# Optimization experiments

Hardware: AMD Instinct MI355X
Metric: run time of the kernel (lower is better)

Reference implementation:

```python
import jax, jax.numpy as jnp
import numpy as np

IN_DIM = 768
HID = 1024          # d_model of Mamba2
CLIP = 512
NG = 4              # ngroups
DS = 64             # d_state
DC = 4              # d_conv
HD = 64             # headdim (Mamba2 default)
DIN = 2 * HID       # d_inner (expand=2)
NH = DIN // HD      # nheads = 32
CONV_DIM = DIN + 2 * NG * DS          # 2560
DINP = 2 * DIN + 2 * NG * DS + NH     # 4640 (d_mlp = 0)
BATCH = 1024
EPS = 1e-5


def setup_inputs() -> dict:
    key = jax.random.key(0)
    ks = jax.random.split(key, 12)
    r = lambda i, shape, s=0.02: jax.random.normal(ks[i], shape, jnp.float32) * s
    return {
        "frame_feat": jax.random.normal(ks[0], (BATCH, IN_DIM), jnp.float32),
        "conv_state": jax.random.normal(ks[1], (BATCH, CONV_DIM, DC), jnp.float32) * 0.1,
        "ssm_state": jax.random.normal(ks[2], (BATCH, NH, HD, DS), jnp.float32) * 0.1,
        "ln_w": jnp.ones((IN_DIM,), jnp.float32),
        "ln_b": jnp.zeros((IN_DIM,), jnp.float32),
        "w_in_gate": r(3, (HID, IN_DIM)),
        "b_in_gate": jnp.zeros((HID,), jnp.float32),
        "w_input_proj": r(4, (HID, IN_DIM)),
        "b_input_proj": jnp.zeros((HID,), jnp.float32),
        "w_in_proj": r(5, (DINP, HID)),                 # Mamba2.in_proj (no bias)
        "conv_w": r(6, (CONV_DIM, DC), 0.1),            # conv1d.weight (d,1,w)->(d,w)
        "conv_b": jnp.zeros((CONV_DIM,), jnp.float32),
        "A_log": jnp.log(jnp.arange(1, NH + 1, dtype=jnp.float32)),
        "Dp": jnp.ones((NH,), jnp.float32),
        "dt_bias": r(7, (NH,), 0.5),
        "norm_w": jnp.ones((DIN,), jnp.float32),        # RMSNormGated weight
        "w_out_proj": r(8, (HID, DIN)),                 # Mamba2.out_proj (no bias)
        "w_out_gate": r(9, (HID, HID)),
        "b_out_gate": jnp.zeros((HID,), jnp.float32),
        "w_proj": r(10, (CLIP, HID)),
        "b_proj": jnp.zeros((CLIP,), jnp.float32),
    }


def reference(frame_feat, conv_state, ssm_state, ln_w, ln_b, w_in_gate, b_in_gate,
              w_input_proj, b_input_proj, w_in_proj, conv_w, conv_b, A_log, Dp,
              dt_bias, norm_w, w_out_proj, w_out_gate, b_out_gate, w_proj, b_proj):
    # ---- pre-LayerNorm ----
    mu = jnp.mean(frame_feat, -1, keepdims=True)
    var = jnp.mean((frame_feat - mu) ** 2, -1, keepdims=True)
    x = (frame_feat - mu) * jax.lax.rsqrt(var + EPS) * ln_w + ln_b
    # ---- gated input projection ----
    gated = (x @ w_input_proj.T + b_input_proj) * jax.nn.sigmoid(x @ w_in_gate.T + b_in_gate)
    # ---- Mamba2.step ----
    zxbcdt = gated @ w_in_proj.T                              # (b, DINP)
    z = zxbcdt[:, :DIN]
    xBC = zxbcdt[:, DIN:DIN + CONV_DIM]
    dt = zxbcdt[:, DIN + CONV_DIM:]                           # (b, NH)
    # causal-conv state update (roll left, append, depthwise dot over window)
    new_conv = jnp.concatenate([conv_state[:, :, 1:], xBC[:, :, None]], axis=-1)
    xBC = jax.nn.silu(jnp.sum(new_conv * conv_w, axis=-1) + conv_b)
    xs = xBC[:, :DIN]
    Bs = xBC[:, DIN:DIN + NG * DS]
    Cs = xBC[:, DIN + NG * DS:]
    # selective state update
    A = -jnp.exp(A_log)                                       # (NH,)
    dt = jax.nn.softplus(dt + dt_bias)                        # (b, NH)
    dA = jnp.exp(dt * A)                                      # (b, NH)
    xh = xs.reshape(-1, NH, HD)                               # (b, h, p)
    hpg = NH // NG
    Bh = jnp.repeat(Bs.reshape(-1, NG, DS), hpg, axis=1)      # (b, h, n)
    Ch = jnp.repeat(Cs.reshape(-1, NG, DS), hpg, axis=1)
    new_ssm = ssm_state * dA[:, :, None, None] + (dt[:, :, None] * xh)[..., None] * Bh[:, :, None, :]
    y = jnp.einsum('bhpn,bhn->bhp', new_ssm, Ch) + Dp[None, :, None] * xh
    # gated group RMSNorm (group_size = DIN // NG, gate applied before norm)
    y = y.reshape(-1, DIN) * jax.nn.silu(z)
    yg = y.reshape(-1, NG, DIN // NG)
    yg = yg * jax.lax.rsqrt(jnp.mean(yg * yg, -1, keepdims=True) + EPS)
    y = yg.reshape(-1, DIN) * norm_w
    ssm_out = y @ w_out_proj.T                                # (b, HID)
    # ---- residual + output gate + projection ----
    out = ssm_out + gated
    out = out * jax.nn.sigmoid(out @ w_out_gate.T + b_out_gate)
    clip_emb = out @ w_proj.T + b_proj
    return clip_emb, new_conv, new_ssm
```

## Files before the change

### kernel.cpp

```cpp
#include <hip/hip_runtime.h>
#include <hip/hip_bf16.h>
#include <math.h>

constexpr int B       = 1024;
constexpr int IN_DIM  = 768;
constexpr int HID     = 1024;
constexpr int CLIP    = 512;
constexpr int NG      = 4;
constexpr int DS      = 64;
constexpr int HD      = 64;
constexpr int DIN     = 2 * HID;
constexpr int NH      = DIN / HD;
constexpr int CONV_DIM = DIN + 2 * NG * DS;
constexpr int DINP    = 2 * DIN + 2 * NG * DS + NH;
constexpr float EPS   = 1e-5f;

__device__ __forceinline__ float sigmoidf_(float v) { return 1.f / (1.f + expf(-v)); }

__global__ __launch_bounds__(256) void ln_kernel(
    const float* __restrict__ in, const float* __restrict__ w,
    const float* __restrict__ bvec, float* __restrict__ out)
{
    int row = blockIdx.x, t = threadIdx.x;
    __shared__ float rs[4], rss[4], stats[2];
    float v[3];
    float s = 0.f, ss = 0.f;
#pragma unroll
    for (int i = 0; i < 3; i++) {
        v[i] = in[row * IN_DIM + i * 256 + t];
        s += v[i]; ss += v[i] * v[i];
    }
    for (int o = 32; o; o >>= 1) { s += __shfl_down(s, o); ss += __shfl_down(ss, o); }
    if ((t & 63) == 0) { rs[t >> 6] = s; rss[t >> 6] = ss; }
    __syncthreads();
    if (t == 0) {
        float S = rs[0] + rs[1] + rs[2] + rs[3];
        float SS = rss[0] + rss[1] + rss[2] + rss[3];
        float mu = S * (1.f / IN_DIM);
        float var = SS * (1.f / IN_DIM) - mu * mu;
        stats[0] = mu; stats[1] = rsqrtf(var + EPS);
    }
    __syncthreads();
    float mu = stats[0], r = stats[1];
#pragma unroll
    for (int i = 0; i < 3; i++) {
        int c = i * 256 + t;
        out[row * IN_DIM + c] = (v[i] - mu) * r * w[c] + bvec[c];
    }
}

template <int EPI>
__global__ __launch_bounds__(256) void gemm_kernel(
    const float* __restrict__ A, const float* __restrict__ W,
    const float* __restrict__ bias, const float* __restrict__ other,
    float* __restrict__ C, int M, int N, int K)
{
    __shared__ float As[16][64];
    __shared__ float Ws[16][64];
    int t = threadIdx.x;
    int tx = t & 15, ty = t >> 4;
    int bm = blockIdx.y * 64, bn = blockIdx.x * 64;
    int lr = t >> 2;
    int lk = (t & 3) * 4;
    const float* Aptr = A + (size_t)(bm + lr) * K + lk;
    const float* Wptr = W + (size_t)(bn + lr) * K + lk;
    bool wvalid = (bn + lr) < N;
    float acc[4][4] = {};
    for (int k0 = 0; k0 < K; k0 += 16) {
        float4 av = *(const float4*)(Aptr + k0);
        float4 wv = wvalid ? *(const float4*)(Wptr + k0) : make_float4(0.f, 0.f, 0.f, 0.f);
        __syncthreads();
        As[lk + 0][lr] = av.x; As[lk + 1][lr] = av.y; As[lk + 2][lr] = av.z; As[lk + 3][lr] = av.w;
        Ws[lk + 0][lr] = wv.x; Ws[lk + 1][lr] = wv.y; Ws[lk + 2][lr] = wv.z; Ws[lk + 3][lr] = wv.w;
        __syncthreads();
#pragma unroll
        for (int kk = 0; kk < 16; kk++) {
            float4 a = *(const float4*)&As[kk][ty * 4];
            float4 b = *(const float4*)&Ws[kk][tx * 4];
            acc[0][0] = fmaf(a.x, b.x, acc[0][0]); acc[0][1] = fmaf(a.x, b.y, acc[0][1]);
            acc[0][2] = fmaf(a.x, b.z, acc[0][2]); acc[0][3] = fmaf(a.x, b.w, acc[0][3]);
            acc[1][0] = fmaf(a.y, b.x, acc[1][0]); acc[1][1] = fmaf(a.y, b.y, acc[1][1]);
            acc[1][2] = fmaf(a.y, b.z, acc[1][2]); acc[1][3] = fmaf(a.y, b.w, acc[1][3]);
            acc[2][0] = fmaf(a.z, b.x, acc[2][0]); acc[2][1] = fmaf(a.z, b.y, acc[2][1]);
            acc[2][2] = fmaf(a.z, b.z, acc[2][2]); acc[2][3] = fmaf(a.z, b.w, acc[2][3]);
            acc[3][0] = fmaf(a.w, b.x, acc[3][0]); acc[3][1] = fmaf(a.w, b.y, acc[3][1]);
            acc[3][2] = fmaf(a.w, b.z, acc[3][2]); acc[3][3] = fmaf(a.w, b.w, acc[3][3]);
        }
    }
    int cn = bn + tx * 4;
    if (cn < N) {
        float4 bz = bias ? *(const float4*)(bias + cn) : make_float4(0.f, 0.f, 0.f, 0.f);
#pragma unroll
        for (int i = 0; i < 4; i++) {
            int rm = bm + ty * 4 + i;
            size_t off = (size_t)rm * N + cn;
            float4 r = make_float4(acc[i][0] + bz.x, acc[i][1] + bz.y,
                                   acc[i][2] + bz.z, acc[i][3] + bz.w);
            if (EPI == 1) {
                float4 o = *(const float4*)(other + off);
                r.x *= sigmoidf_(o.x); r.y *= sigmoidf_(o.y);
                r.z *= sigmoidf_(o.z); r.w *= sigmoidf_(o.w);
            } else if (EPI == 2) {
                float4 o = *(const float4*)(other + off);
                r.x += o.x; r.y += o.y; r.z += o.z; r.w += o.w;
            } else if (EPI == 3) {
                float4 o = *(const float4*)(other + off);
                r.x = o.x * sigmoidf_(r.x); r.y = o.y * sigmoidf_(r.y);
                r.z = o.z * sigmoidf_(r.z); r.w = o.w * sigmoidf_(r.w);
            }
            *(float4*)(C + off) = r;
        }
    }
}

__global__ __launch_bounds__(256) void conv_kernel(
    const float* __restrict__ conv_state, const float* __restrict__ zxbcdt,
    const float* __restrict__ cw, const float* __restrict__ cb,
    float* __restrict__ newconv, float* __restrict__ xbcp)
{
    int idx = blockIdx.x * 256 + threadIdx.x;
    int b = idx / CONV_DIM, c = idx - b * CONV_DIM;
    float4 cs = ((const float4*)conv_state)[idx];
    float xin = zxbcdt[(size_t)b * DINP + DIN + c];
    float4 nc = make_float4(cs.y, cs.z, cs.w, xin);
    ((float4*)newconv)[idx] = nc;
    float4 w = ((const float4*)cw)[c];
    float s = nc.x * w.x + nc.y * w.y + nc.z * w.z + nc.w * w.w + cb[c];
    xbcp[idx] = s * sigmoidf_(s);
}

__global__ __launch_bounds__(256) void dt_kernel(
    const float* __restrict__ zxbcdt, const float* __restrict__ dt_bias,
    const float* __restrict__ A_log, float* __restrict__ dtb, float* __restrict__ dab)
{
    int idx = blockIdx.x * 256 + threadIdx.x;
    int b = idx >> 5, h = idx & 31;
    float raw = zxbcdt[(size_t)b * DINP + DIN + CONV_DIM + h] + dt_bias[h];
    float sp = (raw > 20.f) ? raw : log1pf(expf(raw));
    float A = -expf(A_log[h]);
    dtb[idx] = sp;
    dab[idx] = expf(sp * A);
}

__global__ __launch_bounds__(256) void ssm_kernel(
    const float* __restrict__ ssm_state, const float* __restrict__ xbcp,
    const float* __restrict__ dtb, const float* __restrict__ dab,
    const float* __restrict__ Dp, float* __restrict__ newssm, float* __restrict__ ypre)
{
    int bid = blockIdx.x;
    int b = bid >> 5, h = bid & 31, g = h >> 3;
    int t = threadIdx.x;
    __shared__ float xsh[64];
    __shared__ float4 Bsh[16], Csh[16];
    __shared__ float sc[3];
    if (t < 64) xsh[t] = xbcp[(size_t)b * CONV_DIM + h * 64 + t];
    else if (t < 80)  Bsh[t - 64] = ((const float4*)(xbcp + (size_t)b * CONV_DIM + DIN + g * 64))[t - 64];
    else if (t < 96)  Csh[t - 80] = ((const float4*)(xbcp + (size_t)b * CONV_DIM + DIN + NG * DS + g * 64))[t - 80];
    else if (t == 96) sc[0] = dtb[bid];
    else if (t == 97) sc[1] = dab[bid];
    else if (t == 98) sc[2] = Dp[h];
    __syncthreads();
    float sdt = sc[0], sdA = sc[1], sDp = sc[2];
    const float4* sin4 = (const float4*)ssm_state + (size_t)bid * 1024;
    float4* sout4 = (float4*)newssm + (size_t)bid * 1024;
#pragma unroll
    for (int i = 0; i < 4; i++) {
        int idx = i * 256 + t;
        int p = idx >> 4, n4 = idx & 15;
        float4 s = sin4[idx];
        float4 Bv = Bsh[n4], Cv = Csh[n4];
        float coef = sdt * xsh[p];
        float4 ns;
        ns.x = fmaf(s.x, sdA, coef * Bv.x);
        ns.y = fmaf(s.y, sdA, coef * Bv.y);
        ns.z = fmaf(s.z, sdA, coef * Bv.z);
        ns.w = fmaf(s.w, sdA, coef * Bv.w);
        sout4[idx] = ns;
        float part = ns.x * Cv.x + ns.y * Cv.y + ns.z * Cv.z + ns.w * Cv.w;
        for (int o = 8; o; o >>= 1) part += __shfl_down(part, o);
        if ((t & 15) == 0) ypre[(size_t)b * DIN + h * 64 + p] = part + sDp * xsh[p];
    }
}

__global__ __launch_bounds__(128) void gn_kernel(
    const float* __restrict__ ypre, const float* __restrict__ zxbcdt,
    const float* __restrict__ nw, float* __restrict__ yfin)
{
    int bg = blockIdx.x;
    int b = bg >> 2, g = bg & 3;
    int t = threadIdx.x;
    int col = g * 512 + t * 4;
    float4 yv = *(const float4*)(ypre + (size_t)b * DIN + col);
    float4 zv = *(const float4*)(zxbcdt + (size_t)b * DINP + col);
    float4 y2;
    y2.x = yv.x * zv.x * sigmoidf_(zv.x);
    y2.y = yv.y * zv.y * sigmoidf_(zv.y);
    y2.z = yv.z * zv.z * sigmoidf_(zv.z);
    y2.w = yv.w * zv.w * sigmoidf_(zv.w);
    float ss = y2.x * y2.x + y2.y * y2.y + y2.z * y2.z + y2.w * y2.w;
    for (int o = 32; o; o >>= 1) ss += __shfl_down(ss, o);
    __shared__ float red[2]; __shared__ float rfac;
    if ((t & 63) == 0) red[t >> 6] = ss;
    __syncthreads();
    if (t == 0) rfac = rsqrtf((red[0] + red[1]) * (1.f / 512.f) + EPS);
    __syncthreads();
    float r = rfac;
    float4 w4 = *(const float4*)(nw + col);
    float4 o4 = make_float4(y2.x * r * w4.x, y2.y * r * w4.y, y2.z * r * w4.z, y2.w * r * w4.w);
    *(float4*)(yfin + (size_t)b * DIN + col) = o4;
}

extern "C" void kernel_launch(void* const* d_in, const int* in_sizes, int n_in,
                              void* d_out, int out_size, void* d_ws, size_t ws_size,
                              hipStream_t stream)
{
    const float* frame_feat   = (const float*)d_in[0];
    const float* conv_state   = (const float*)d_in[1];
    const float* ssm_state    = (const float*)d_in[2];
    const float* ln_w         = (const float*)d_in[3];
    const float* ln_b         = (const float*)d_in[4];
    const float* w_in_gate    = (const float*)d_in[5];
    const float* b_in_gate    = (const float*)d_in[6];
    const float* w_input_proj = (const float*)d_in[7];
    const float* b_input_proj = (const float*)d_in[8];
    const float* w_in_proj    = (const float*)d_in[9];
    const float* conv_w       = (const float*)d_in[10];
    const float* conv_b       = (const float*)d_in[11];
    const float* A_log        = (const float*)d_in[12];
    const float* Dp           = (const float*)d_in[13];
    const float* dt_bias      = (const float*)d_in[14];
    const float* norm_w       = (const float*)d_in[15];
    const float* w_out_proj   = (const float*)d_in[16];
    const float* w_out_gate   = (const float*)d_in[17];
    const float* b_out_gate   = (const float*)d_in[18];
    const float* w_proj       = (const float*)d_in[19];
    const float* b_proj       = (const float*)d_in[20];

    float* ws = (float*)d_ws;
    float* x      = ws + 0;
    float* g1     = ws + 786432;
    float* gated  = ws + 1835008;
    float* zxbcdt = ws + 2883584;
    float* xbcp   = ws + 7634944;
    float* dtb    = ws + 10256384;
    float* dab    = ws + 10289152;
    float* ypre   = ws + 10321920;
    float* yfin   = ws + 12419072;
    float* outpre = ws + 14516224;
    float* outv   = ws + 15564800;

    float* out     = (float*)d_out;
    float* clip    = out;
    float* newconv = out + (size_t)B * CLIP;
    float* newssm  = newconv + (size_t)B * CONV_DIM * 4;

    ln_kernel<<<B, 256, 0, stream>>>(frame_feat, ln_w, ln_b, x);
    gemm_kernel<0><<<dim3(HID / 64, B / 64), 256, 0, stream>>>(
        x, w_in_gate, b_in_gate, nullptr, g1, B, HID, IN_DIM);
    gemm_kernel<1><<<dim3(HID / 64, B / 64), 256, 0, stream>>>(
        x, w_input_proj, b_input_proj, g1, gated, B, HID, IN_DIM);
    gemm_kernel<0><<<dim3((DINP + 63) / 64, B / 64), 256, 0, stream>>>(
        gated, w_in_proj, nullptr, nullptr, zxbcdt, B, DINP, HID);
    conv_kernel<<<(B * CONV_DIM) / 256, 256, 0, stream>>>(
        conv_state, zxbcdt, conv_w, conv_b, newconv, xbcp);
    dt_kernel<<<(B * NH) / 256, 256, 0, stream>>>(zxbcdt, dt_bias, A_log, dtb, dab);
    ssm_kernel<<<B * NH, 256, 0, stream>>>(ssm_state, xbcp, dtb, dab, Dp, newssm, ypre);
    gn_kernel<<<B * NG, 128, 0, stream>>>(ypre, zxbcdt, norm_w, yfin);
    gemm_kernel<2><<<dim3(HID / 64, B / 64), 256, 0, stream>>>(
        yfin, w_out_proj, nullptr, gated, outpre, B, HID, DIN);
    gemm_kernel<3><<<dim3(HID / 64, B / 64), 256, 0, stream>>>(
        outpre, w_out_gate, b_out_gate, outpre, outv, B, HID, HID);
    gemm_kernel<0><<<dim3(CLIP / 64, B / 64), 256, 0, stream>>>(
        outv, w_proj, b_proj, nullptr, clip, B, CLIP, HID);
}
```

Before: 1.439 ms.

## Replace FP32 SIMT GEMMs with split-bf16 MFMA GEMMs and fuse input-gate projections

```diff
diff --git a/kernel.cpp b/kernel.cpp
--- a/kernel.cpp
+++ b/kernel.cpp
@@ -1,5 +1,4 @@
 #include <hip/hip_runtime.h>
-#include <hip/hip_bf16.h>
 #include <math.h>
 
 constexpr int B       = 1024;
@@ -15,11 +14,30 @@
 constexpr int DINP    = 2 * DIN + 2 * NG * DS + NH;
 constexpr float EPS   = 1e-5f;
 
+typedef __attribute__((ext_vector_type(8))) short bf16x8;
+typedef __attribute__((ext_vector_type(4))) float f32x4;
+typedef __attribute__((ext_vector_type(8))) unsigned short u16x8;
+
 __device__ __forceinline__ float sigmoidf_(float v) { return 1.f / (1.f + expf(-v)); }
+
+__device__ __forceinline__ unsigned short f2bf(float f) {
+    unsigned int u = __float_as_uint(f);
+    u += 0x7fffu + ((u >> 16) & 1u);
+    return (unsigned short)(u >> 16);
+}
+__device__ __forceinline__ float bf2f(unsigned short h) {
+    return __uint_as_float(((unsigned int)h) << 16);
+}
+
+__device__ __forceinline__ void gload_lds16(const unsigned short* g, short* l) {
+    __builtin_amdgcn_global_load_lds(
+        (const __attribute__((address_space(1))) unsigned int*)(const void*)g,
+        (__attribute__((address_space(3))) unsigned int*)(void*)l, 16, 0, 0);
+}
 
 __global__ __launch_bounds__(256) void ln_kernel(
     const float* __restrict__ in, const float* __restrict__ w,
-    const float* __restrict__ bvec, float* __restrict__ out)
+    const float* __restrict__ bvec, unsigned short* __restrict__ x2)
 {
     int row = blockIdx.x, t = threadIdx.x;
     __shared__ float rs[4], rss[4], stats[2];
@@ -45,72 +63,158 @@
 #pragma unroll
     for (int i = 0; i < 3; i++) {
         int c = i * 256 + t;
-        out[row * IN_DIM + c] = (v[i] - mu) * r * w[c] + bvec[c];
-    }
-}
-
-template <int EPI>
-__global__ __launch_bounds__(256) void gemm_kernel(
-    const float* __restrict__ A, const float* __restrict__ W,
+        float val = (v[i] - mu) * r * w[c] + bvec[c];
+        unsigned short h = f2bf(val);
+        unsigned short lo = f2bf(val - bf2f(h));
+        x2[(size_t)row * 1536 + c] = h;
+        x2[(size_t)row * 1536 + 768 + c] = lo;
+    }
+}
+
+__global__ __launch_bounds__(256) void convert_split(
+    const float* __restrict__ in, unsigned short* __restrict__ out, int K)
+{
+    size_t idx = (size_t)(blockIdx.x * 256 + threadIdx.x) * 8;
+    int r = (int)(idx / K);
+    int c = (int)(idx - (size_t)r * K);
+    float4 a = *(const float4*)(in + idx);
+    float4 b = *(const float4*)(in + idx + 4);
+    float v[8] = {a.x, a.y, a.z, a.w, b.x, b.y, b.z, b.w};
+    u16x8 h, l;
+#pragma unroll
+    for (int j = 0; j < 8; j++) {
+        unsigned short hh = f2bf(v[j]);
+        h[j] = hh;
+        l[j] = f2bf(v[j] - bf2f(hh));
+    }
+    size_t ro = (size_t)r * 2 * K;
+    *(u16x8*)(out + ro + c)     = h;
+    *(u16x8*)(out + ro + K + c) = l;
+}
+
+template <int EPI, bool WF32, bool SPLIT>
+__global__ __launch_bounds__(256) void gemm_mfma(
+    const unsigned short* __restrict__ A2, const unsigned short* __restrict__ W2,
     const float* __restrict__ bias, const float* __restrict__ other,
-    float* __restrict__ C, int M, int N, int K)
-{
-    __shared__ float As[16][64];
-    __shared__ float Ws[16][64];
-    int t = threadIdx.x;
-    int tx = t & 15, ty = t >> 4;
-    int bm = blockIdx.y * 64, bn = blockIdx.x * 64;
-    int lr = t >> 2;
-    int lk = (t & 3) * 4;
-    const float* Aptr = A + (size_t)(bm + lr) * K + lk;
-    const float* Wptr = W + (size_t)(bn + lr) * K + lk;
-    bool wvalid = (bn + lr) < N;
-    float acc[4][4] = {};
-    for (int k0 = 0; k0 < K; k0 += 16) {
-        float4 av = *(const float4*)(Aptr + k0);
-        float4 wv = wvalid ? *(const float4*)(Wptr + k0) : make_float4(0.f, 0.f, 0.f, 0.f);
+    float* __restrict__ C, unsigned short* __restrict__ C2,
+    int M, int N, int K)
+{
+    __shared__ short As[2][128 * 64];
+    __shared__ short Ws[2][128 * 64];
+    const int t = threadIdx.x;
+    const int wid = t >> 6, lane = t & 63;
+    const int bm = blockIdx.y * 128, bn = blockIdx.x * 128;
+    const int wm = wid >> 1, wn = wid & 1;
+    const int l15 = lane & 15, l16 = lane >> 4;
+    const size_t str = 2 * (size_t)K;
+    const int Nm1 = N - 1;
+    const int rsub = lane >> 3;
+    const int scb  = 8 * ((lane & 7) ^ (lane >> 3));
+
+    f32x4 acc[4][4];
+#pragma unroll
+    for (int i = 0; i < 4; i++)
+#pragma unroll
+        for (int j = 0; j < 4; j++) acc[i][j] = (f32x4){0.f, 0.f, 0.f, 0.f};
+
+    const int K3 = 3 * K;
+    const int nt = K3 / 64;
+
+    auto stage = [&](int bufidx, int k0) {
+        const int Acol = (k0 < 2 * K) ? k0 : k0 - 2 * K;
+        const int Wcol = (k0 < K) ? k0 : k0 - K;
+        short* Ab = &As[bufidx][0];
+        short* Wb = &Ws[bufidx][0];
+#pragma unroll
+        for (int c = 0; c < 4; c++) {
+            int chunk = c * 4 + wid;
+            int row = chunk * 8 + rsub;
+            int rowW = bn + row; if (rowW > Nm1) rowW = Nm1;
+            gload_lds16(A2 + (size_t)(bm + row) * str + Acol + scb, Ab + chunk * 512);
+            gload_lds16(W2 + (size_t)rowW * str + Wcol + scb, Wb + chunk * 512);
+        }
+    };
+
+    stage(0, 0);
+    __syncthreads();
+    int cur = 0;
+    for (int it = 0; it < nt; ++it) {
+        if (it + 1 < nt) stage(cur ^ 1, (it + 1) * 64);
+        const short* Ab = &As[cur][0];
+        const short* Wb = &Ws[cur][0];
+#pragma unroll
+        for (int kk = 0; kk < 2; kk++) {
+            const int ke = kk * 32 + l16 * 8;
+            bf16x8 av[4], bv[4];
+#pragma unroll
+            for (int mi = 0; mi < 4; mi++) {
+                int r = wm * 64 + mi * 16 + l15;
+                av[mi] = *(const bf16x8*)(Ab + r * 64 + (ke ^ ((r & 7) << 3)));
+            }
+#pragma unroll
+            for (int ni = 0; ni < 4; ni++) {
+                int r = wn * 64 + ni * 16 + l15;
+                bv[ni] = *(const bf16x8*)(Wb + r * 64 + (ke ^ ((r & 7) << 3)));
+            }
+#pragma unroll
+            for (int mi = 0; mi < 4; mi++)
+#pragma unroll
+                for (int ni = 0; ni < 4; ni++)
+                    acc[mi][ni] = __builtin_amdgcn_mfma_f32_16x16x32_bf16(
+                        av[mi], bv[ni], acc[mi][ni], 0, 0, 0);
+        }
         __syncthreads();
-        As[lk + 0][lr] = av.x; As[lk + 1][lr] = av.y; As[lk + 2][lr] = av.z; As[lk + 3][lr] = av.w;
-        Ws[lk + 0][lr] = wv.x; Ws[lk + 1][lr] = wv.y; Ws[lk + 2][lr] = wv.z; Ws[lk + 3][lr] = wv.w;
-        __syncthreads();
-#pragma unroll
-        for (int kk = 0; kk < 16; kk++) {
-            float4 a = *(const float4*)&As[kk][ty * 4];
-            float4 b = *(const float4*)&Ws[kk][tx * 4];
-            acc[0][0] = fmaf(a.x, b.x, acc[0][0]); acc[0][1] = fmaf(a.x, b.y, acc[0][1]);
-            acc[0][2] = fmaf(a.x, b.z, acc[0][2]); acc[0][3] = fmaf(a.x, b.w, acc[0][3]);
-            acc[1][0] = fmaf(a.y, b.x, acc[1][0]); acc[1][1] = fmaf(a.y, b.y, acc[1][1]);
-            acc[1][2] = fmaf(a.y, b.z, acc[1][2]); acc[1][3] = fmaf(a.y, b.w, acc[1][3]);
-            acc[2][0] = fmaf(a.z, b.x, acc[2][0]); acc[2][1] = fmaf(a.z, b.y, acc[2][1]);
-            acc[2][2] = fmaf(a.z, b.z, acc[2][2]); acc[2][3] = fmaf(a.z, b.w, acc[2][3]);
-            acc[3][0] = fmaf(a.w, b.x, acc[3][0]); acc[3][1] = fmaf(a.w, b.y, acc[3][1]);
-            acc[3][2] = fmaf(a.w, b.z, acc[3][2]); acc[3][3] = fmaf(a.w, b.w, acc[3][3]);
+        cur ^= 1;
+    }
+
+#pragma unroll
+    for (int ni = 0; ni < 4; ni++) {
+        const int cg = bn + wn * 64 + ni * 16 + l15;
+        if (cg >= N) continue;
+        const float bz = bias ? bias[cg] : 0.f;
+#pragma unroll
+        for (int mi = 0; mi < 4; mi++) {
+            const int rbase = bm + wm * 64 + mi * 16 + l16 * 4;
+#pragma unroll
+            for (int rr = 0; rr < 4; rr++) {
+                const size_t off = (size_t)(rbase + rr) * N + cg;
+                float val = acc[mi][ni][rr] + bz;
+                if (EPI == 2) val += other[off];
+                else if (EPI == 3) val = other[off] * sigmoidf_(val);
+                if (WF32) C[off] = val;
+                if (SPLIT) {
+                    unsigned short h = f2bf(val);
+                    unsigned short lo = f2bf(val - bf2f(h));
+                    size_t o2 = (size_t)(rbase + rr) * (2 * (size_t)N) + cg;
+                    C2[o2] = h; C2[o2 + N] = lo;
+                }
+            }
         }
     }
-    int cn = bn + tx * 4;
-    if (cn < N) {
-        float4 bz = bias ? *(const float4*)(bias + cn) : make_float4(0.f, 0.f, 0.f, 0.f);
-#pragma unroll
-        for (int i = 0; i < 4; i++) {
-            int rm = bm + ty * 4 + i;
-            size_t off = (size_t)rm * N + cn;
-            float4 r = make_float4(acc[i][0] + bz.x, acc[i][1] + bz.y,
-                                   acc[i][2] + bz.z, acc[i][3] + bz.w);
-            if (EPI == 1) {
-                float4 o = *(const float4*)(other + off);
-                r.x *= sigmoidf_(o.x); r.y *= sigmoidf_(o.y);
-                r.z *= sigmoidf_(o.z); r.w *= sigmoidf_(o.w);
-            } else if (EPI == 2) {
-                float4 o = *(const float4*)(other + off);
-                r.x += o.x; r.y += o.y; r.z += o.z; r.w += o.w;
-            } else if (EPI == 3) {
-                float4 o = *(const float4*)(other + off);
-                r.x = o.x * sigmoidf_(r.x); r.y = o.y * sigmoidf_(r.y);
-                r.z = o.z * sigmoidf_(r.z); r.w = o.w * sigmoidf_(r.w);
-            }
-            *(float4*)(C + off) = r;
-        }
-    }
+}
+
+__global__ __launch_bounds__(256) void gate_mul_kernel(
+    const float* __restrict__ gpcat, const float* __restrict__ bg,
+    const float* __restrict__ bp, float* __restrict__ gated,
+    unsigned short* __restrict__ gated2)
+{
+    int idx = blockIdx.x * 256 + threadIdx.x;
+    int b = idx >> 8, j4 = (idx & 255) * 4;
+    float4 g = *(const float4*)(gpcat + (size_t)b * 2048 + j4);
+    float4 p = *(const float4*)(gpcat + (size_t)b * 2048 + 1024 + j4);
+    float4 bgv = *(const float4*)(bg + j4);
+    float4 bpv = *(const float4*)(bp + j4);
+    float4 r;
+    r.x = (p.x + bpv.x) * sigmoidf_(g.x + bgv.x);
+    r.y = (p.y + bpv.y) * sigmoidf_(g.y + bgv.y);
+    r.z = (p.z + bpv.z) * sigmoidf_(g.z + bgv.z);
+    r.w = (p.w + bpv.w) * sigmoidf_(g.w + bgv.w);
+    *(float4*)(gated + (size_t)b * 1024 + j4) = r;
+    ushort4 h = make_ushort4(f2bf(r.x), f2bf(r.y), f2bf(r.z), f2bf(r.w));
+    ushort4 l = make_ushort4(f2bf(r.x - bf2f(h.x)), f2bf(r.y - bf2f(h.y)),
+                             f2bf(r.z - bf2f(h.z)), f2bf(r.w - bf2f(h.w)));
+    *(ushort4*)(gated2 + (size_t)b * 2048 + j4) = h;
+    *(ushort4*)(gated2 + (size_t)b * 2048 + 1024 + j4) = l;
 }
 
 __global__ __launch_bounds__(256) void conv_kernel(
@@ -184,7 +288,7 @@
 
 __global__ __launch_bounds__(128) void gn_kernel(
     const float* __restrict__ ypre, const float* __restrict__ zxbcdt,
-    const float* __restrict__ nw, float* __restrict__ yfin)
+    const float* __restrict__ nw, unsigned short* __restrict__ yfin2)
 {
     int bg = blockIdx.x;
     int b = bg >> 2, g = bg & 3;
@@ -207,7 +311,11 @@
     float r = rfac;
     float4 w4 = *(const float4*)(nw + col);
     float4 o4 = make_float4(y2.x * r * w4.x, y2.y * r * w4.y, y2.z * r * w4.z, y2.w * r * w4.w);
-    *(float4*)(yfin + (size_t)b * DIN + col) = o4;
+    ushort4 h = make_ushort4(f2bf(o4.x), f2bf(o4.y), f2bf(o4.z), f2bf(o4.w));
+    ushort4 l = make_ushort4(f2bf(o4.x - bf2f(h.x)), f2bf(o4.y - bf2f(h.y)),
+                             f2bf(o4.z - bf2f(h.z)), f2bf(o4.w - bf2f(h.w)));
+    *(ushort4*)(yfin2 + (size_t)b * 4096 + col) = h;
+    *(ushort4*)(yfin2 + (size_t)b * 4096 + 2048 + col) = l;
 }
 
 extern "C" void kernel_launch(void* const* d_in, const int* in_sizes, int n_in,
@@ -237,39 +345,52 @@
     const float* b_proj       = (const float*)d_in[20];
 
     float* ws = (float*)d_ws;
-    float* x      = ws + 0;
-    float* g1     = ws + 786432;
-    float* gated  = ws + 1835008;
-    float* zxbcdt = ws + 2883584;
-    float* xbcp   = ws + 7634944;
-    float* dtb    = ws + 10256384;
-    float* dab    = ws + 10289152;
-    float* ypre   = ws + 10321920;
-    float* yfin   = ws + 12419072;
-    float* outpre = ws + 14516224;
-    float* outv   = ws + 15564800;
+    float* gpcat  = ws + 0;
+    float* ypre   = gpcat;
+    float* gated  = ws + 2097152;
+    float* zxbcdt = ws + 3145728;
+    float* xbcp   = ws + 7897088;
+    float* dtb    = ws + 10518528;
+    float* dab    = ws + 10551296;
+    float* outpre = ws + 10584064;
+    unsigned short* u = (unsigned short*)(ws + 11632640);
+    unsigned short* x2      = u + 0;
+    unsigned short* wgp2    = u + 1572864;
+    unsigned short* gated2  = u + 4718592;
+    unsigned short* winp2   = u + 6815744;
+    unsigned short* yfin2   = u + 16318464;
+    unsigned short* woutp2  = u + 20512768;
+    unsigned short* outpre2 = u + 24707072;
+    unsigned short* woutg2  = u + 26804224;
+    unsigned short* outv2   = u + 28901376;
+    unsigned short* wproj2  = u + 30998528;
 
     float* out     = (float*)d_out;
     float* clip    = out;
     float* newconv = out + (size_t)B * CLIP;
     float* newssm  = newconv + (size_t)B * CONV_DIM * 4;
 
-    ln_kernel<<<B, 256, 0, stream>>>(frame_feat, ln_w, ln_b, x);
-    gemm_kernel<0><<<dim3(HID / 64, B / 64), 256, 0, stream>>>(
-        x, w_in_gate, b_in_gate, nullptr, g1, B, HID, IN_DIM);
-    gemm_kernel<1><<<dim3(HID / 64, B / 64), 256, 0, stream>>>(
-        x, w_input_proj, b_input_proj, g1, gated, B, HID, IN_DIM);
-    gemm_kernel<0><<<dim3((DINP + 63) / 64, B / 64), 256, 0, stream>>>(
-        gated, w_in_proj, nullptr, nullptr, zxbcdt, B, DINP, HID);
+    ln_kernel<<<B, 256, 0, stream>>>(frame_feat, ln_w, ln_b, x2);
+    convert_split<<<384, 256, 0, stream>>>(w_in_gate, wgp2, IN_DIM);
+    convert_split<<<384, 256, 0, stream>>>(w_input_proj, wgp2 + (size_t)1024 * 1536, IN_DIM);
+    convert_split<<<2320, 256, 0, stream>>>(w_in_proj, winp2, HID);
+    convert_split<<<1024, 256, 0, stream>>>(w_out_proj, woutp2, DIN);
+    convert_split<<<512, 256, 0, stream>>>(w_out_gate, woutg2, HID);
+    convert_split<<<256, 256, 0, stream>>>(w_proj, wproj2, HID);
+    gemm_mfma<0, true, false><<<dim3(16, 8), 256, 0, stream>>>(
+        x2, wgp2, nullptr, nullptr, gpcat, nullptr, B, 2 * HID, IN_DIM);
+    gate_mul_kernel<<<1024, 256, 0, stream>>>(gpcat, b_in_gate, b_input_proj, gated, gated2);
+    gemm_mfma<0, true, false><<<dim3(37, 8), 256, 0, stream>>>(
+        gated2, winp2, nullptr, nullptr, zxbcdt, nullptr, B, DINP, HID);
     conv_kernel<<<(B * CONV_DIM) / 256, 256, 0, stream>>>(
         conv_state, zxbcdt, conv_w, conv_b, newconv, xbcp);
     dt_kernel<<<(B * NH) / 256, 256, 0, stream>>>(zxbcdt, dt_bias, A_log, dtb, dab);
     ssm_kernel<<<B * NH, 256, 0, stream>>>(ssm_state, xbcp, dtb, dab, Dp, newssm, ypre);
-    gn_kernel<<<B * NG, 128, 0, stream>>>(ypre, zxbcdt, norm_w, yfin);
-    gemm_kernel<2><<<dim3(HID / 64, B / 64), 256, 0, stream>>>(
-        yfin, w_out_proj, nullptr, gated, outpre, B, HID, DIN);
-    gemm_kernel<3><<<dim3(HID / 64, B / 64), 256, 0, stream>>>(
-        outpre, w_out_gate, b_out_gate, outpre, outv, B, HID, HID);
-    gemm_kernel<0><<<dim3(CLIP / 64, B / 64), 256, 0, stream>>>(
-        outv, w_proj, b_proj, nullptr, clip, B, CLIP, HID);
-}
+    gn_kernel<<<B * NG, 128, 0, stream>>>(ypre, zxbcdt, norm_w, yfin2);
+    gemm_mfma<2, true, true><<<dim3(8, 8), 256, 0, stream>>>(
+        yfin2, woutp2, nullptr, gated, outpre, outpre2, B, HID, DIN);
+    gemm_mfma<3, false, true><<<dim3(8, 8), 256, 0, stream>>>(
+        outpre2, woutg2, b_out_gate, outpre, nullptr, outv2, B, HID, HID);
+    gemm_mfma<0, true, false><<<dim3(4, 8), 256, 0, stream>>>(
+        outv2, wproj2, b_proj, nullptr, clip, nullptr, B, CLIP, HID);
+}
```

Result: faster. 1.325 ms (-7.9%).
